# Kernel tuning notes

Measured on AMD Instinct MI355X. Metric: run time of the kernel, lower is better.

The kernel has to match this reference:

```python
import jax, jax.numpy as jnp
import numpy as np
from jax import lax

N, D, H, O = 16384, 512, 1024, 512
G, E, K = 3, 4, 2
ALPHA = 0.01


def setup_inputs() -> dict:
    key = jax.random.key(0)
    ks = jax.random.split(key, 16)

    def lin(k, out_d, in_d):
        s = 1.0 / np.sqrt(in_d)
        return jax.random.uniform(k, (out_d, in_d), jnp.float32, -s, s)

    x = jax.random.normal(ks[0], (N, D), jnp.float32)
    Wm = lin(ks[1], G, D)
    bm = jnp.zeros((G,), jnp.float32)
    # group routers stacked: [G, E, D]
    Wr = jax.random.uniform(ks[2], (G, E, D), jnp.float32, -1 / np.sqrt(D), 1 / np.sqrt(D))
    br = jnp.zeros((G, E), jnp.float32)
    # expert params stacked over (group, expert)
    W1 = jax.random.uniform(ks[3], (G, E, H, D), jnp.float32, -1 / np.sqrt(D), 1 / np.sqrt(D))
    b1 = jnp.zeros((G, E, H), jnp.float32)
    W2 = jax.random.uniform(ks[4], (G, E, H, H), jnp.float32, -1 / np.sqrt(H), 1 / np.sqrt(H))
    b2 = jnp.zeros((G, E, H), jnp.float32)
    Wp = jax.random.uniform(ks[5], (G, E, H, D), jnp.float32, -1 / np.sqrt(D), 1 / np.sqrt(D))
    bp = jnp.zeros((G, E, H), jnp.float32)
    W3 = jax.random.uniform(ks[6], (G, E, O, H), jnp.float32, -1 / np.sqrt(H), 1 / np.sqrt(H))
    b3 = jnp.zeros((G, E, O), jnp.float32)
    return {"x": x, "Wm": Wm, "bm": bm, "Wr": Wr, "br": br,
            "W1": W1, "b1": b1, "W2": W2, "b2": b2,
            "Wp": Wp, "bp": bp, "W3": W3, "b3": b3}


def _expert(x, W1, b1, W2, b2, Wp, bp, W3, b3):
    # residual MLP (dropout in eval mode => identity)
    h = jax.nn.relu(x @ W1.T + b1)
    h = h @ W2.T + b2
    ident = x @ Wp.T + bp  # projection (input_dim != hidden_dim)
    h = jax.nn.relu(h + ident)
    return h @ W3.T + b3


def reference(x, Wm, bm, Wr, br, W1, b1, W2, b2, Wp, bp, W3, b3):
    n = x.shape[0]
    # ---- meta (top-1 group) routing ----
    meta_logits = x @ Wm.T + bm                         # [N, G]
    g = jnp.argmax(meta_logits, axis=1)                 # top-1 group per token
    pm = jax.nn.softmax(meta_logits, axis=1).mean(0)    # [G]
    aux = ALPHA * G * jnp.sum(pm * pm)
    # ---- per-group router logits, gathered for each token's group ----
    logits_all = jnp.einsum('nd,ged->nge', x, Wr) + br  # [N, G, E]
    sel = jnp.take_along_axis(logits_all, g[:, None, None], axis=1)[:, 0, :]  # [N, E]
    # ---- group-level load-balancing aux loss (over tokens in each group) ----
    probs = jax.nn.softmax(sel, axis=-1)                # [N, E]
    onehot_g = (g[:, None] == jnp.arange(G)[None, :])   # [N, G] bool
    cnt = onehot_g.sum(0)                               # [G]
    mean_g = (onehot_g.astype(x.dtype).T @ probs) / jnp.maximum(cnt, 1)[:, None].astype(x.dtype)
    aux = aux + jnp.sum(jnp.where(cnt > 0, ALPHA * E * jnp.sum(mean_g * mean_g, -1), 0.0))
    # ---- top-k expert weights within selected group (softmax over the k logits) ----
    vals, idx = lax.top_k(sel, K)                       # [N, K]
    w = jax.nn.softmax(vals, axis=-1)                   # [N, K]
    cw = jnp.zeros((n, E), x.dtype).at[jnp.arange(n)[:, None], idx].set(w)   # [N, E]
    combine = cw[:, None, :] * onehot_g[:, :, None].astype(x.dtype)          # [N, G, E]
    # ---- expert compute + combine (loop over the fixed small set of experts) ----
    out = jnp.zeros((n, O), x.dtype)
    for gi in range(G):
        for e in range(E):
            y = _expert(x, W1[gi, e], b1[gi, e], W2[gi, e], b2[gi, e],
                        Wp[gi, e], bp[gi, e], W3[gi, e], b3[gi, e])
            out = out + combine[:, gi, e:e + 1] * y
    return out, aux
```

## Files before the change

kernel.cpp:

```cpp
#include <hip/hip_runtime.h>
#include <hip/hip_bf16.h>

#define N_TOK 16384
#define DDIM  512
#define HDIM  1024
#define ODIM  512
#define NG    3
#define NE    4
#define NGE   12
#define TASK_CAP 272

typedef __bf16 bf16x8 __attribute__((ext_vector_type(8)));
typedef float  f32x4  __attribute__((ext_vector_type(4)));
typedef unsigned int u32;

__device__ __forceinline__ void gld_lds16(const void* gsrc, void* ldst) {
    __builtin_amdgcn_global_load_lds(
        (const __attribute__((address_space(1))) u32*)gsrc,
        (__attribute__((address_space(3))) u32*)ldst, 16, 0, 0);
}

static constexpr size_t OFF_WSLOT = 512;
static constexpr size_t OFF_ELIST = OFF_WSLOT + (size_t)N_TOK*2*4;
static constexpr size_t OFF_TASK  = 917504;
static constexpr size_t OFF_XBF   = 1048576;
static constexpr size_t OFF_W1    = OFF_XBF + (size_t)N_TOK*DDIM*2;
static constexpr size_t OFF_W2    = OFF_W1  + (size_t)NGE*HDIM*DDIM*2;
static constexpr size_t OFF_WP    = OFF_W2  + (size_t)NGE*HDIM*HDIM*2;
static constexpr size_t OFF_W3    = OFF_WP  + (size_t)NGE*HDIM*DDIM*2;
static constexpr size_t OFF_H1    = OFF_W3  + (size_t)NGE*ODIM*HDIM*2;
static constexpr size_t OFF_U     = OFF_H1  + (size_t)N_TOK*2*HDIM*2;
static constexpr size_t OFF_Y     = OFF_U   + (size_t)N_TOK*2*HDIM*2;
static constexpr size_t WS_NEED   = OFF_Y   + (size_t)N_TOK*2*ODIM*2;

__global__ void cast_all_k(const float* __restrict__ x,  const float* __restrict__ w1,
                           const float* __restrict__ w2, const float* __restrict__ wp,
                           const float* __restrict__ w3,
                           __bf16* xbf, __bf16* w1b, __bf16* w2b, __bf16* wpb, __bf16* w3b) {
    int tid = blockIdx.x * blockDim.x + threadIdx.x;
    int stride = gridDim.x * blockDim.x;
    auto seg = [&](const float* __restrict__ s, __bf16* __restrict__ d, int n4) {
        const float4* s4 = (const float4*)s;
        uint2* d4 = (uint2*)d;
        for (int i = tid; i < n4; i += stride) {
            float4 v = s4[i];
            union { __bf16 h[4]; uint2 u; } o;
            o.h[0] = (__bf16)v.x; o.h[1] = (__bf16)v.y;
            o.h[2] = (__bf16)v.z; o.h[3] = (__bf16)v.w;
            d4[i] = o.u;
        }
    };
    seg(x,  xbf, N_TOK*DDIM/4);
    seg(w1, w1b, NGE*HDIM*DDIM/4);
    seg(w2, w2b, NGE*HDIM*HDIM/4);
    seg(wp, wpb, NGE*HDIM*DDIM/4);
    seg(w3, w3b, NGE*ODIM*HDIM/4);
}

__global__ __launch_bounds__(256) void routing_k(
        const float* __restrict__ x,  const float* __restrict__ Wm,
        const float* __restrict__ bm, const float* __restrict__ Wr,
        const float* __restrict__ br,
        float* pmsum, float* psum, int* cnt, int* ecount,
        int* elist, float* wslot) {
    __shared__ float lpm[NG];
    __shared__ float lpsum[NGE];
    __shared__ int   lcnt[NG];
    __shared__ int   lec[NGE];
    __shared__ int   lbase[NGE];
    __shared__ int   lentry[NGE][64];

    int tid = threadIdx.x;
    if (tid < NG)  { lpm[tid] = 0.f; lcnt[tid] = 0; }
    if (tid < NGE) { lpsum[tid] = 0.f; lec[tid] = 0; }
    __syncthreads();

    int wid = tid >> 6, lane = tid & 63;

    #pragma unroll 1
    for (int i = 0; i < 16; ++i) {
        int t = blockIdx.x * 64 + i * 4 + wid;

        const float4* xr = (const float4*)(x + (size_t)t * DDIM);
        float4 xa = xr[lane*2], xb = xr[lane*2+1];

        float meta[NG];
        #pragma unroll
        for (int gi = 0; gi < NG; ++gi) {
            const float4* w = (const float4*)(Wm + gi*DDIM);
            float4 wa = w[lane*2], wb = w[lane*2+1];
            float s = xa.x*wa.x + xa.y*wa.y + xa.z*wa.z + xa.w*wa.w
                    + xb.x*wb.x + xb.y*wb.y + xb.z*wb.z + xb.w*wb.w;
            #pragma unroll
            for (int off = 32; off > 0; off >>= 1) s += __shfl_xor(s, off);
            meta[gi] = s + bm[gi];
        }
        int g = 0;
        if (meta[1] > meta[g]) g = 1;
        if (meta[2] > meta[g]) g = 2;

        float mm = fmaxf(meta[0], fmaxf(meta[1], meta[2]));
        float e0 = expf(meta[0]-mm), e1 = expf(meta[1]-mm), e2 = expf(meta[2]-mm);
        float inv = 1.f / (e0 + e1 + e2);

        float sel[NE];
        #pragma unroll
        for (int e = 0; e < NE; ++e) {
            const float4* w = (const float4*)(Wr + (size_t)(g*NE + e)*DDIM);
            float4 wa = w[lane*2], wb = w[lane*2+1];
            float s = xa.x*wa.x + xa.y*wa.y + xa.z*wa.z + xa.w*wa.w
                    + xb.x*wb.x + xb.y*wb.y + xb.z*wb.z + xb.w*wb.w;
            #pragma unroll
            for (int off = 32; off > 0; off >>= 1) s += __shfl_xor(s, off);
            sel[e] = s + br[g*NE + e];
        }
        float ms = fmaxf(fmaxf(sel[0],sel[1]), fmaxf(sel[2],sel[3]));
        float pe[NE]; float ss = 0.f;
        #pragma unroll
        for (int e = 0; e < NE; ++e) { pe[e] = expf(sel[e]-ms); ss += pe[e]; }
        float invs = 1.f / ss;

        int i0 = 0;
        #pragma unroll
        for (int e = 1; e < NE; ++e) if (sel[e] > sel[i0]) i0 = e;
        int i1 = (i0 == 0) ? 1 : 0;
        #pragma unroll
        for (int e = 0; e < NE; ++e) if (e != i0 && sel[e] > sel[i1]) i1 = e;
        float ew = expf(sel[i1] - sel[i0]);
        float wden = 1.f / (1.f + ew);

        if (lane == 0) {
            atomicAdd(&lpm[0], e0*inv);
            atomicAdd(&lpm[1], e1*inv);
            atomicAdd(&lpm[2], e2*inv);
            #pragma unroll
            for (int e = 0; e < NE; ++e) atomicAdd(&lpsum[g*NE + e], pe[e]*invs);
            atomicAdd(&lcnt[g], 1);
            int ee0 = g*NE + i0, ee1 = g*NE + i1;
            int p0 = atomicAdd(&lec[ee0], 1);
            lentry[ee0][p0] = t*2;
            int p1 = atomicAdd(&lec[ee1], 1);
            lentry[ee1][p1] = t*2 + 1;
            wslot[t*2]   = wden;
            wslot[t*2+1] = ew * wden;
        }
    }
    __syncthreads();

    if (tid < NG)  { atomicAdd(pmsum + tid, lpm[tid]); atomicAdd(cnt + tid, lcnt[tid]); }
    if (tid < NGE) { atomicAdd(psum + tid, lpsum[tid]);
                     lbase[tid] = atomicAdd(ecount + tid, lec[tid]); }
    __syncthreads();

    for (int e = wid; e < NGE; e += 4) {
        int c = lec[e], base = lbase[e];
        for (int j = lane; j < c; j += 64)
            elist[e*N_TOK + base + j] = lentry[e][j];
    }
}

__global__ void finalize_aux_k(const float* pmsum, const float* psum, const int* cnt,
                               const int* ecount, int2* tasks, int* ntasks,
                               float* outAux) {
    if (threadIdx.x != 0 || blockIdx.x != 0) return;
    float s = 0.f;
    for (int i = 0; i < NG; ++i) { float p = pmsum[i] / (float)N_TOK; s += p*p; }
    float aux = 0.01f * NG * s;
    for (int gg = 0; gg < NG; ++gg) {
        int c = cnt[gg];
        if (c > 0) {
            float s2 = 0.f;
            for (int e = 0; e < NE; ++e) { float m = psum[gg*NE+e] / (float)c; s2 += m*m; }
            aux += 0.01f * NE * s2;
        }
    }
    *outAux = aux;
    int nt = 0;
    for (int ge = 0; ge < NGE; ++ge) {
        int c = ecount[ge];
        for (int m0 = 0; m0 < c; m0 += 128) tasks[nt++] = make_int2(ge, m0);
    }
    *ntasks = nt;
}

template<int NDIM, bool RELU, bool TWOPASS>
__global__ __launch_bounds__(256) void expert_gemm_k(
        const __bf16* __restrict__ A1, int shift1, int k1, const __bf16* __restrict__ B1,
        const __bf16* __restrict__ A2, int shift2, int k2, const __bf16* __restrict__ B2,
        const float* __restrict__ bias1, const float* __restrict__ bias2,
        __bf16* __restrict__ Out,
        const int* __restrict__ ecount, const int* __restrict__ elist,
        const int2* __restrict__ tasks, const int* __restrict__ ntasks) {
    constexpr int NPAN = NDIM / 128;
    int bid = blockIdx.x;
    int grp = bid / (8 * NPAN);
    int rem = bid % (8 * NPAN);
    int panel = rem >> 3;
    int task  = grp * 8 + (rem & 7);
    if (task >= *ntasks) return;
    int2 tk = tasks[task];
    int ge = tk.x, m0 = tk.y;
    int cntE = ecount[ge];
    int n0 = panel * 128;

    __shared__ __align__(16) char ldsA[2][16384];
    __shared__ __align__(16) char ldsB[2][16384];
    __shared__ int ents[128];

    int tid = threadIdx.x;
    if (tid < 128) {
        int r = m0 + tid;
        if (r >= cntE) r = cntE - 1;
        ents[tid] = elist[ge*N_TOK + r];
    }
    __syncthreads();

    int lane = tid & 63, wv = tid >> 6;
    int wm = wv >> 1, wn = wv & 1;
    int lr = lane & 15, lg = lane >> 4;
    int rl = lane >> 3;
    int csw = (lane & 7) ^ rl;
    int rsw = lr & 7;

    const char* sA1[4]; const char* sB1[4];
    const char* sA2[4]; const char* sB2[4];
    size_t rowB1 = (size_t)k1 * 2;
    const char* Bb1 = (const char*)(B1 + (size_t)ge * NDIM * k1) + (size_t)n0 * rowB1;
    #pragma unroll
    for (int j = 0; j < 4; ++j) {
        int r = wv*32 + j*8 + rl;
        sA1[j] = (const char*)A1 + (size_t)(ents[r] >> shift1) * rowB1 + (size_t)csw*16;
        sB1[j] = Bb1 + (size_t)r * rowB1 + (size_t)csw*16;
    }
    if constexpr (TWOPASS) {
        size_t rowB2 = (size_t)k2 * 2;
        const char* Bb2 = (const char*)(B2 + (size_t)ge * NDIM * k2) + (size_t)n0 * rowB2;
        #pragma unroll
        for (int j = 0; j < 4; ++j) {
            int r = wv*32 + j*8 + rl;
            sA2[j] = (const char*)A2 + (size_t)(ents[r] >> shift2) * rowB2 + (size_t)csw*16;
            sB2[j] = Bb2 + (size_t)r * rowB2 + (size_t)csw*16;
        }
    }

    int nk1 = k1 >> 6;
    int nk  = TWOPASS ? nk1 + (k2 >> 6) : nk1;

    auto stage = [&](int s) {
        int b = s & 1;
        if (!TWOPASS || s < nk1) {
            size_t ko = (size_t)s << 7;
            #pragma unroll
            for (int j = 0; j < 4; ++j) {
                gld_lds16(sA1[j] + ko, ldsA[b] + (wv*4 + j)*1024);
                gld_lds16(sB1[j] + ko, ldsB[b] + (wv*4 + j)*1024);
            }
        } else {
            size_t ko = (size_t)(s - nk1) << 7;
            #pragma unroll
            for (int j = 0; j < 4; ++j) {
                gld_lds16(sA2[j] + ko, ldsA[b] + (wv*4 + j)*1024);
                gld_lds16(sB2[j] + ko, ldsB[b] + (wv*4 + j)*1024);
            }
        }
    };

    f32x4 acc[4][4] = {};

    stage(0);
    __syncthreads();

    #pragma unroll 1
    for (int s = 0; s < nk; ++s) {
        if (s + 1 < nk) stage(s + 1);
        const char* bA = ldsA[s & 1];
        const char* bB = ldsB[s & 1];
        #pragma unroll
        for (int kk = 0; kk < 2; ++kk) {
            bf16x8 av[4], bv[4];
            #pragma unroll
            for (int mi = 0; mi < 4; ++mi) {
                int ar = wm*64 + mi*16 + lr;
                av[mi] = *(const bf16x8*)(bA + ar*128 + ((((kk*4+lg) ^ rsw)) << 4));
            }
            #pragma unroll
            for (int ni = 0; ni < 4; ++ni) {
                int br_ = wn*64 + ni*16 + lr;
                bv[ni] = *(const bf16x8*)(bB + br_*128 + ((((kk*4+lg) ^ rsw)) << 4));
            }
            #pragma unroll
            for (int mi = 0; mi < 4; ++mi)
                #pragma unroll
                for (int ni = 0; ni < 4; ++ni)
                    acc[mi][ni] = __builtin_amdgcn_mfma_f32_16x16x32_bf16(
                        av[mi], bv[ni], acc[mi][ni], 0, 0, 0);
        }
        __syncthreads();
    }

    #pragma unroll
    for (int ni = 0; ni < 4; ++ni) {
        int col = n0 + wn*64 + ni*16 + lr;
        float b = bias1[(size_t)ge*NDIM + col];
        if constexpr (TWOPASS) b += bias2[(size_t)ge*NDIM + col];
        #pragma unroll
        for (int mi = 0; mi < 4; ++mi) {
            #pragma unroll
            for (int j = 0; j < 4; ++j) {
                int rloc = wm*64 + mi*16 + lg*4 + j;
                if (m0 + rloc < cntE) {
                    float v = acc[mi][ni][j] + b;
                    if constexpr (RELU) v = fmaxf(v, 0.f);
                    Out[(size_t)ents[rloc] * NDIM + col] = (__bf16)v;
                }
            }
        }
    }
}

__global__ void combine_k(const __bf16* __restrict__ Y, const float* __restrict__ wslot,
                          float* __restrict__ out) {
    int idx = blockIdx.x * blockDim.x + threadIdx.x;
    int t = idx >> 6;
    int o = (idx & 63) * 8;
    bf16x8 y0 = *(const bf16x8*)(Y + (size_t)(2*t)   * ODIM + o);
    bf16x8 y1 = *(const bf16x8*)(Y + (size_t)(2*t+1) * ODIM + o);
    float w0 = wslot[2*t], w1 = wslot[2*t+1];
    float4 r0, r1;
    r0.x = w0*(float)y0[0] + w1*(float)y1[0];
    r0.y = w0*(float)y0[1] + w1*(float)y1[1];
    r0.z = w0*(float)y0[2] + w1*(float)y1[2];
    r0.w = w0*(float)y0[3] + w1*(float)y1[3];
    r1.x = w0*(float)y0[4] + w1*(float)y1[4];
    r1.y = w0*(float)y0[5] + w1*(float)y1[5];
    r1.z = w0*(float)y0[6] + w1*(float)y1[6];
    r1.w = w0*(float)y0[7] + w1*(float)y1[7];
    float* op = out + (size_t)t * ODIM + o;
    ((float4*)op)[0] = r0;
    ((float4*)op)[1] = r1;
}

extern "C" void kernel_launch(void* const* d_in, const int* in_sizes, int n_in,
                              void* d_out, int out_size, void* d_ws, size_t ws_size,
                              hipStream_t stream) {
    const float* x  = (const float*)d_in[0];
    const float* Wm = (const float*)d_in[1];
    const float* bm = (const float*)d_in[2];
    const float* Wr = (const float*)d_in[3];
    const float* br = (const float*)d_in[4];
    const float* W1 = (const float*)d_in[5];
    const float* b1 = (const float*)d_in[6];
    const float* W2 = (const float*)d_in[7];
    const float* b2 = (const float*)d_in[8];
    const float* Wp = (const float*)d_in[9];
    const float* bp = (const float*)d_in[10];
    const float* W3 = (const float*)d_in[11];
    const float* b3 = (const float*)d_in[12];

    if (ws_size < WS_NEED) return;

    char* ws = (char*)d_ws;
    float* outp = (float*)d_out;

    float* pmsum  = (float*)ws;
    float* psum   = (float*)ws + 4;
    int*   cnt    = (int*)ws + 16;
    int*   ecount = (int*)ws + 20;
    int*   ntasks = (int*)ws + 34;
    float* wslot  = (float*)(ws + OFF_WSLOT);
    int*   elist  = (int*)(ws + OFF_ELIST);
    int2*  tasks  = (int2*)(ws + OFF_TASK);
    __bf16* xbf = (__bf16*)(ws + OFF_XBF);
    __bf16* w1b = (__bf16*)(ws + OFF_W1);
    __bf16* w2b = (__bf16*)(ws + OFF_W2);
    __bf16* wpb = (__bf16*)(ws + OFF_WP);
    __bf16* w3b = (__bf16*)(ws + OFF_W3);
    __bf16* H1  = (__bf16*)(ws + OFF_H1);
    __bf16* U   = (__bf16*)(ws + OFF_U);
    __bf16* Y   = (__bf16*)(ws + OFF_Y);

    hipMemsetAsync(d_ws, 0, 512, stream);

    cast_all_k<<<4096, 256, 0, stream>>>(x, W1, W2, Wp, W3, xbf, w1b, w2b, wpb, w3b);

    routing_k<<<256, 256, 0, stream>>>(x, Wm, bm, Wr, br,
                                       pmsum, psum, cnt, ecount, elist, wslot);

    finalize_aux_k<<<1, 64, 0, stream>>>(pmsum, psum, cnt, ecount, tasks, ntasks,
                                         outp + (size_t)N_TOK*ODIM);

    expert_gemm_k<HDIM, true, false><<<TASK_CAP*(HDIM/128), 256, 0, stream>>>(
        xbf, 1, DDIM, w1b, nullptr, 0, 0, nullptr, b1, nullptr, H1,
        ecount, elist, tasks, ntasks);

    expert_gemm_k<HDIM, true, true><<<TASK_CAP*(HDIM/128), 256, 0, stream>>>(
        H1, 0, HDIM, w2b, xbf, 1, DDIM, wpb, b2, bp, U,
        ecount, elist, tasks, ntasks);

    expert_gemm_k<ODIM, false, false><<<TASK_CAP*(ODIM/128), 256, 0, stream>>>(
        U, 0, HDIM, w3b, nullptr, 0, 0, nullptr, b3, nullptr, Y,
        ecount, elist, tasks, ntasks);

    combine_k<<<4096, 256, 0, stream>>>(Y, wslot, outp);
}
```

Before: 454.0 us.

## Enlarge expert GEMM tile to 256 rows with 4-stage async LDS pipeline

The expert GEMM block grows to 512 threads and a 256x128 output tile, with row tasks chunked by 256 instead of 128. The K loop now streams 32-wide slices through a 4-deep LDS ring using direct global-to-LDS loads, explicit vmcnt waits and raw barriers. MFMA sections run at raised wave priority, and the LDS swizzle is redone for 64-byte rows. The aim is more reuse of weight tiles per block and more loads in flight to hide memory latency. The cost is two barriers for every 16 MFMAs, more padding waste on partial 256-row tasks, and fewer blocks to spread across CUs.

```diff
diff --git a/kernel.cpp b/kernel.cpp
--- a/kernel.cpp
+++ b/kernel.cpp
@@ -8,7 +8,7 @@
 #define NG    3
 #define NE    4
 #define NGE   12
-#define TASK_CAP 272
+#define TASK_CAP 144
 
 typedef __bf16 bf16x8 __attribute__((ext_vector_type(8)));
 typedef float  f32x4  __attribute__((ext_vector_type(4)));
@@ -178,13 +178,13 @@
     int nt = 0;
     for (int ge = 0; ge < NGE; ++ge) {
         int c = ecount[ge];
-        for (int m0 = 0; m0 < c; m0 += 128) tasks[nt++] = make_int2(ge, m0);
+        for (int m0 = 0; m0 < c; m0 += 256) tasks[nt++] = make_int2(ge, m0);
     }
     *ntasks = nt;
 }
 
 template<int NDIM, bool RELU, bool TWOPASS>
-__global__ __launch_bounds__(256) void expert_gemm_k(
+__global__ __launch_bounds__(512) void expert_gemm_k(
         const __bf16* __restrict__ A1, int shift1, int k1, const __bf16* __restrict__ B1,
         const __bf16* __restrict__ A2, int shift2, int k2, const __bf16* __restrict__ B2,
         const float* __restrict__ bias1, const float* __restrict__ bias2,
@@ -203,12 +203,12 @@
     int cntE = ecount[ge];
     int n0 = panel * 128;
 
-    __shared__ __align__(16) char ldsA[2][16384];
-    __shared__ __align__(16) char ldsB[2][16384];
-    __shared__ int ents[128];
+    __shared__ __align__(16) char ldsA[4][16384];
+    __shared__ __align__(16) char ldsB[4][8192];
+    __shared__ int ents[256];
 
     int tid = threadIdx.x;
-    if (tid < 128) {
+    if (tid < 256) {
         int r = m0 + tid;
         if (r >= cntE) r = cntE - 1;
         ents[tid] = elist[ge*N_TOK + r];
@@ -218,84 +218,85 @@
     int lane = tid & 63, wv = tid >> 6;
     int wm = wv >> 1, wn = wv & 1;
     int lr = lane & 15, lg = lane >> 4;
-    int rl = lane >> 3;
-    int csw = (lane & 7) ^ rl;
-    int rsw = lr & 7;
-
-    const char* sA1[4]; const char* sB1[4];
-    const char* sA2[4]; const char* sB2[4];
+    int cr = lane >> 2;
+    int cg = (lane & 3) ^ ((lane >> 3) & 3);
+
     size_t rowB1 = (size_t)k1 * 2;
-    const char* Bb1 = (const char*)(B1 + (size_t)ge * NDIM * k1) + (size_t)n0 * rowB1;
-    #pragma unroll
-    for (int j = 0; j < 4; ++j) {
-        int r = wv*32 + j*8 + rl;
-        sA1[j] = (const char*)A1 + (size_t)(ents[r] >> shift1) * rowB1 + (size_t)csw*16;
-        sB1[j] = Bb1 + (size_t)r * rowB1 + (size_t)csw*16;
-    }
+    const char* pA10 = (const char*)A1 + (size_t)(ents[32*wv + cr]      >> shift1) * rowB1 + cg*16;
+    const char* pA11 = (const char*)A1 + (size_t)(ents[32*wv + 16 + cr] >> shift1) * rowB1 + cg*16;
+    const char* pB1  = (const char*)(B1 + (size_t)(ge*NDIM + n0 + 16*wv + cr) * k1) + cg*16;
+    const char* pA20 = nullptr; const char* pA21 = nullptr; const char* pB2 = nullptr;
+    int nk1 = k1 >> 6;
+    int H = 2 * nk1;
     if constexpr (TWOPASS) {
         size_t rowB2 = (size_t)k2 * 2;
-        const char* Bb2 = (const char*)(B2 + (size_t)ge * NDIM * k2) + (size_t)n0 * rowB2;
-        #pragma unroll
-        for (int j = 0; j < 4; ++j) {
-            int r = wv*32 + j*8 + rl;
-            sA2[j] = (const char*)A2 + (size_t)(ents[r] >> shift2) * rowB2 + (size_t)csw*16;
-            sB2[j] = Bb2 + (size_t)r * rowB2 + (size_t)csw*16;
-        }
-    }
-
-    int nk1 = k1 >> 6;
-    int nk  = TWOPASS ? nk1 + (k2 >> 6) : nk1;
-
-    auto stage = [&](int s) {
-        int b = s & 1;
-        if (!TWOPASS || s < nk1) {
-            size_t ko = (size_t)s << 7;
+        pA20 = (const char*)A2 + (size_t)(ents[32*wv + cr]      >> shift2) * rowB2 + cg*16;
+        pA21 = (const char*)A2 + (size_t)(ents[32*wv + 16 + cr] >> shift2) * rowB2 + cg*16;
+        pB2  = (const char*)(B2 + (size_t)(ge*NDIM + n0 + 16*wv + cr) * k2) + cg*16;
+        H += 2 * (k2 >> 6);
+    }
+
+    auto stageH = [&](int h) {
+        int q = h & 3;
+        char* dA = ldsA[q] + 2*wv*1024;
+        char* dB = ldsB[q] + wv*1024;
+        if (!TWOPASS || h < 2*nk1) {
+            size_t off = (size_t)h << 6;
+            gld_lds16(pA10 + off, dA);
+            gld_lds16(pA11 + off, dA + 1024);
+            gld_lds16(pB1  + off, dB);
+        } else {
+            size_t off = (size_t)(h - 2*nk1) << 6;
+            gld_lds16(pA20 + off, dA);
+            gld_lds16(pA21 + off, dA + 1024);
+            gld_lds16(pB2  + off, dB);
+        }
+    };
+
+    f32x4 acc[4][4] = {};
+
+    stageH(0); stageH(1); stageH(2);
+
+    #pragma unroll 1
+    for (int p = 0; p < H; ++p) {
+        if (p + 3 < H) {
+            stageH(p + 3);
+            asm volatile("s_waitcnt vmcnt(9)" ::: "memory");
+        } else {
+            int remh = H - 1 - p;
+            if (remh == 2)      asm volatile("s_waitcnt vmcnt(6)" ::: "memory");
+            else if (remh == 1) asm volatile("s_waitcnt vmcnt(3)" ::: "memory");
+            else                asm volatile("s_waitcnt vmcnt(0)" ::: "memory");
+        }
+        __builtin_amdgcn_sched_barrier(0);
+        __builtin_amdgcn_s_barrier();
+        __builtin_amdgcn_sched_barrier(0);
+
+        int q = p & 3;
+        bf16x8 av[4], bv[4];
+        #pragma unroll
+        for (int mi = 0; mi < 4; ++mi) {
+            int ar = wm*64 + mi*16 + lr;
+            av[mi] = *(const bf16x8*)(ldsA[q] + ar*64 + ((lg ^ ((ar >> 1) & 3)) << 4));
+        }
+        #pragma unroll
+        for (int ni = 0; ni < 4; ++ni) {
+            int br_ = wn*64 + ni*16 + lr;
+            bv[ni] = *(const bf16x8*)(ldsB[q] + br_*64 + ((lg ^ ((br_ >> 1) & 3)) << 4));
+        }
+        asm volatile("s_waitcnt lgkmcnt(0)" ::: "memory");
+        __builtin_amdgcn_sched_barrier(0);
+        __builtin_amdgcn_s_setprio(1);
+        #pragma unroll
+        for (int mi = 0; mi < 4; ++mi)
             #pragma unroll
-            for (int j = 0; j < 4; ++j) {
-                gld_lds16(sA1[j] + ko, ldsA[b] + (wv*4 + j)*1024);
-                gld_lds16(sB1[j] + ko, ldsB[b] + (wv*4 + j)*1024);
-            }
-        } else {
-            size_t ko = (size_t)(s - nk1) << 7;
-            #pragma unroll
-            for (int j = 0; j < 4; ++j) {
-                gld_lds16(sA2[j] + ko, ldsA[b] + (wv*4 + j)*1024);
-                gld_lds16(sB2[j] + ko, ldsB[b] + (wv*4 + j)*1024);
-            }
-        }
-    };
-
-    f32x4 acc[4][4] = {};
-
-    stage(0);
-    __syncthreads();
-
-    #pragma unroll 1
-    for (int s = 0; s < nk; ++s) {
-        if (s + 1 < nk) stage(s + 1);
-        const char* bA = ldsA[s & 1];
-        const char* bB = ldsB[s & 1];
-        #pragma unroll
-        for (int kk = 0; kk < 2; ++kk) {
-            bf16x8 av[4], bv[4];
-            #pragma unroll
-            for (int mi = 0; mi < 4; ++mi) {
-                int ar = wm*64 + mi*16 + lr;
-                av[mi] = *(const bf16x8*)(bA + ar*128 + ((((kk*4+lg) ^ rsw)) << 4));
-            }
-            #pragma unroll
-            for (int ni = 0; ni < 4; ++ni) {
-                int br_ = wn*64 + ni*16 + lr;
-                bv[ni] = *(const bf16x8*)(bB + br_*128 + ((((kk*4+lg) ^ rsw)) << 4));
-            }
-            #pragma unroll
-            for (int mi = 0; mi < 4; ++mi)
-                #pragma unroll
-                for (int ni = 0; ni < 4; ++ni)
-                    acc[mi][ni] = __builtin_amdgcn_mfma_f32_16x16x32_bf16(
-                        av[mi], bv[ni], acc[mi][ni], 0, 0, 0);
-        }
-        __syncthreads();
+            for (int ni = 0; ni < 4; ++ni)
+                acc[mi][ni] = __builtin_amdgcn_mfma_f32_16x16x32_bf16(
+                    av[mi], bv[ni], acc[mi][ni], 0, 0, 0);
+        __builtin_amdgcn_s_setprio(0);
+        __builtin_amdgcn_sched_barrier(0);
+        __builtin_amdgcn_s_barrier();
+        __builtin_amdgcn_sched_barrier(0);
     }
 
     #pragma unroll
@@ -389,15 +390,15 @@
     finalize_aux_k<<<1, 64, 0, stream>>>(pmsum, psum, cnt, ecount, tasks, ntasks,
                                          outp + (size_t)N_TOK*ODIM);
 
-    expert_gemm_k<HDIM, true, false><<<TASK_CAP*(HDIM/128), 256, 0, stream>>>(
+    expert_gemm_k<HDIM, true, false><<<TASK_CAP*(HDIM/128), 512, 0, stream>>>(
         xbf, 1, DDIM, w1b, nullptr, 0, 0, nullptr, b1, nullptr, H1,
         ecount, elist, tasks, ntasks);
 
-    expert_gemm_k<HDIM, true, true><<<TASK_CAP*(HDIM/128), 256, 0, stream>>>(
+    expert_gemm_k<HDIM, true, true><<<TASK_CAP*(HDIM/128), 512, 0, stream>>>(
         H1, 0, HDIM, w2b, xbf, 1, DDIM, wpb, b2, bp, U,
         ecount, elist, tasks, ntasks);
 
-    expert_gemm_k<ODIM, false, false><<<TASK_CAP*(ODIM/128), 256, 0, stream>>>(
+    expert_gemm_k<ODIM, false, false><<<TASK_CAP*(ODIM/128), 512, 0, stream>>>(
         U, 0, HDIM, w3b, nullptr, 0, 0, nullptr, b3, nullptr, Y,
         ecount, elist, tasks, ntasks);
 
```

Measured after the change: 695.2 us. 53.1% more time.

## Replace LDS double-buffered staging with direct global-to-register MFMA operand loads

Applied to the files above, without the earlier changes.

Removes the global_load_lds double-buffered shared-memory pipeline from the grouped expert GEMM. Each wave now loads its A and B MFMA fragments straight from global memory into registers and relies on L1/L2 for reuse between waves. This drops the LDS traffic and the block-wide barriers, but operands shared across waves are fetched redundantly and the explicit prefetch overlap is lost.

```diff
diff --git a/kernel.cpp b/kernel.cpp
--- a/kernel.cpp
+++ b/kernel.cpp
@@ -12,13 +12,6 @@
 
 typedef __bf16 bf16x8 __attribute__((ext_vector_type(8)));
 typedef float  f32x4  __attribute__((ext_vector_type(4)));
-typedef unsigned int u32;
-
-__device__ __forceinline__ void gld_lds16(const void* gsrc, void* ldst) {
-    __builtin_amdgcn_global_load_lds(
-        (const __attribute__((address_space(1))) u32*)gsrc,
-        (__attribute__((address_space(3))) u32*)ldst, 16, 0, 0);
-}
 
 static constexpr size_t OFF_WSLOT = 512;
 static constexpr size_t OFF_ELIST = OFF_WSLOT + (size_t)N_TOK*2*4;
@@ -203,10 +196,7 @@
     int cntE = ecount[ge];
     int n0 = panel * 128;
 
-    __shared__ __align__(16) char ldsA[2][16384];
-    __shared__ __align__(16) char ldsB[2][16384];
     __shared__ int ents[128];
-
     int tid = threadIdx.x;
     if (tid < 128) {
         int r = m0 + tid;
@@ -218,76 +208,26 @@
     int lane = tid & 63, wv = tid >> 6;
     int wm = wv >> 1, wn = wv & 1;
     int lr = lane & 15, lg = lane >> 4;
-    int rl = lane >> 3;
-    int csw = (lane & 7) ^ rl;
-    int rsw = lr & 7;
-
-    const char* sA1[4]; const char* sB1[4];
-    const char* sA2[4]; const char* sB2[4];
-    size_t rowB1 = (size_t)k1 * 2;
-    const char* Bb1 = (const char*)(B1 + (size_t)ge * NDIM * k1) + (size_t)n0 * rowB1;
-    #pragma unroll
-    for (int j = 0; j < 4; ++j) {
-        int r = wv*32 + j*8 + rl;
-        sA1[j] = (const char*)A1 + (size_t)(ents[r] >> shift1) * rowB1 + (size_t)csw*16;
-        sB1[j] = Bb1 + (size_t)r * rowB1 + (size_t)csw*16;
-    }
-    if constexpr (TWOPASS) {
-        size_t rowB2 = (size_t)k2 * 2;
-        const char* Bb2 = (const char*)(B2 + (size_t)ge * NDIM * k2) + (size_t)n0 * rowB2;
-        #pragma unroll
-        for (int j = 0; j < 4; ++j) {
-            int r = wv*32 + j*8 + rl;
-            sA2[j] = (const char*)A2 + (size_t)(ents[r] >> shift2) * rowB2 + (size_t)csw*16;
-            sB2[j] = Bb2 + (size_t)r * rowB2 + (size_t)csw*16;
-        }
-    }
-
-    int nk1 = k1 >> 6;
-    int nk  = TWOPASS ? nk1 + (k2 >> 6) : nk1;
-
-    auto stage = [&](int s) {
-        int b = s & 1;
-        if (!TWOPASS || s < nk1) {
-            size_t ko = (size_t)s << 7;
-            #pragma unroll
-            for (int j = 0; j < 4; ++j) {
-                gld_lds16(sA1[j] + ko, ldsA[b] + (wv*4 + j)*1024);
-                gld_lds16(sB1[j] + ko, ldsB[b] + (wv*4 + j)*1024);
-            }
-        } else {
-            size_t ko = (size_t)(s - nk1) << 7;
-            #pragma unroll
-            for (int j = 0; j < 4; ++j) {
-                gld_lds16(sA2[j] + ko, ldsA[b] + (wv*4 + j)*1024);
-                gld_lds16(sB2[j] + ko, ldsB[b] + (wv*4 + j)*1024);
-            }
-        }
-    };
 
     f32x4 acc[4][4] = {};
 
-    stage(0);
-    __syncthreads();
-
-    #pragma unroll 1
-    for (int s = 0; s < nk; ++s) {
-        if (s + 1 < nk) stage(s + 1);
-        const char* bA = ldsA[s & 1];
-        const char* bB = ldsB[s & 1];
-        #pragma unroll
-        for (int kk = 0; kk < 2; ++kk) {
+    {
+        size_t rowA = (size_t)k1 * 2;
+        const char* pa[4]; const char* pb[4];
+        #pragma unroll
+        for (int mi = 0; mi < 4; ++mi)
+            pa[mi] = (const char*)A1 + (size_t)(ents[wm*64 + mi*16 + lr] >> shift1) * rowA + lg*16;
+        #pragma unroll
+        for (int ni = 0; ni < 4; ++ni)
+            pb[ni] = (const char*)(B1 + (size_t)(ge*NDIM + n0 + wn*64 + ni*16 + lr) * k1) + lg*16;
+
+        #pragma unroll 2
+        for (int k0 = 0; k0 < k1; k0 += 32) {
             bf16x8 av[4], bv[4];
             #pragma unroll
-            for (int mi = 0; mi < 4; ++mi) {
-                int ar = wm*64 + mi*16 + lr;
-                av[mi] = *(const bf16x8*)(bA + ar*128 + ((((kk*4+lg) ^ rsw)) << 4));
-            }
-            #pragma unroll
-            for (int ni = 0; ni < 4; ++ni) {
-                int br_ = wn*64 + ni*16 + lr;
-                bv[ni] = *(const bf16x8*)(bB + br_*128 + ((((kk*4+lg) ^ rsw)) << 4));
-            }
+            for (int mi = 0; mi < 4; ++mi) av[mi] = *(const bf16x8*)(pa[mi] + (size_t)k0*2);
+            #pragma unroll
+            for (int ni = 0; ni < 4; ++ni) bv[ni] = *(const bf16x8*)(pb[ni] + (size_t)k0*2);
             #pragma unroll
             for (int mi = 0; mi < 4; ++mi)
                 #pragma unroll
@@ -295,7 +235,32 @@
                     acc[mi][ni] = __builtin_amdgcn_mfma_f32_16x16x32_bf16(
                         av[mi], bv[ni], acc[mi][ni], 0, 0, 0);
         }
-        __syncthreads();
+    }
+
+    if constexpr (TWOPASS) {
+        size_t rowA = (size_t)k2 * 2;
+        const char* pa[4]; const char* pb[4];
+        #pragma unroll
+        for (int mi = 0; mi < 4; ++mi)
+            pa[mi] = (const char*)A2 + (size_t)(ents[wm*64 + mi*16 + lr] >> shift2) * rowA + lg*16;
+        #pragma unroll
+        for (int ni = 0; ni < 4; ++ni)
+            pb[ni] = (const char*)(B2 + (size_t)(ge*NDIM + n0 + wn*64 + ni*16 + lr) * k2) + lg*16;
+
+        #pragma unroll 2
+        for (int k0 = 0; k0 < k2; k0 += 32) {
+            bf16x8 av[4], bv[4];
+            #pragma unroll
+            for (int mi = 0; mi < 4; ++mi) av[mi] = *(const bf16x8*)(pa[mi] + (size_t)k0*2);
+            #pragma unroll
+            for (int ni = 0; ni < 4; ++ni) bv[ni] = *(const bf16x8*)(pb[ni] + (size_t)k0*2);
+            #pragma unroll
+            for (int mi = 0; mi < 4; ++mi)
+                #pragma unroll
+                for (int ni = 0; ni < 4; ++ni)
+                    acc[mi][ni] = __builtin_amdgcn_mfma_f32_16x16x32_bf16(
+                        av[mi], bv[ni], acc[mi][ni], 0, 0, 0);
+        }
     }
 
     #pragma unroll
```

Result: slower. 835.9 us (+84.1%).
